# Optimization experiments

Hardware: AMD Instinct MI355X
Metric: run time of the kernel (lower is better)

Reference implementation:

```python
import jax, jax.numpy as jnp
import numpy as np

N = 50000   # num_embs = num nodes
E = 800000  # num edges
D = 256     # feature dim
L = 4       # num layers
EPS = 1e-5


def setup_inputs() -> dict:
    key = jax.random.key(0)
    ks = jax.random.split(key, 8)
    scale = 1.0 / np.sqrt(D)
    return {
        "x": jax.random.normal(ks[0], (N, D), dtype=jnp.float32),  # ignored by forward
        "edge_index": jax.random.randint(ks[1], (2, E), 0, N, dtype=jnp.int32),
        "edge_weight": jax.random.uniform(ks[2], (E,), dtype=jnp.float32),
        "emb_weight": jax.random.normal(ks[3], (N, D), dtype=jnp.float32),
        "ln_w": jnp.ones((L, D), dtype=jnp.float32),
        "ln_b": jnp.zeros((L, D), dtype=jnp.float32),
        "conv_w": jax.random.normal(ks[4], (L, D, D), dtype=jnp.float32) * scale,
        "conv_b": jnp.zeros((L, D), dtype=jnp.float32),
        "post_w": jax.random.normal(ks[5], (D, D), dtype=jnp.float32) * scale,
        "post_b": jnp.zeros((D,), dtype=jnp.float32),
    }


def _layer_norm(h, w, b):
    mu = jnp.mean(h, axis=-1, keepdims=True)
    var = jnp.mean(jnp.square(h - mu), axis=-1, keepdims=True)
    return (h - mu) * jax.lax.rsqrt(var + EPS) * w + b


def reference(x, edge_index, edge_weight, emb_weight, ln_w, ln_b, conv_w, conv_b, post_w, post_b):
    # GCNConv semantics (PyG defaults): add self-loops (weight 1), symmetric norm.
    loop = jnp.arange(N, dtype=edge_index.dtype)
    src = jnp.concatenate([edge_index[0], loop])
    dst = jnp.concatenate([edge_index[1], loop])
    w = jnp.concatenate([edge_weight, jnp.ones((N,), edge_weight.dtype)])
    deg = jax.ops.segment_sum(w, dst, num_segments=N)
    dinv = jnp.where(deg > 0, jax.lax.rsqrt(jnp.maximum(deg, 1e-12)), 0.0)
    coef = (dinv[src] * w * dinv[dst])[:, None]  # [E+N, 1]

    h = emb_weight  # forward ignores x; cond_emb is None
    for i in range(L):
        z = _layer_norm(h, ln_w[i], ln_b[i])          # node LayerNorm
        zw = z @ conv_w[i]                             # linear transform
        agg = jax.ops.segment_sum(coef * zw[src], dst, num_segments=N)
        z = agg + conv_b[i]
        z = jax.nn.gelu(z, approximate=False)          # torch GELU is exact
        h = z + h                                      # residual (dropout=0)
    return h @ post_w + post_b
```

## Files before the change

### kernel.cpp

```cpp
#include <hip/hip_runtime.h>
#include <hip/hip_bf16.h>

#define N_NODES 50000
#define N_EDGES 800000
#define DIM     256
#define NLAYERS 4
#define EPS     1e-5f
#define SCAN_B  196
#define MASK40  ((1ULL << 40) - 1)
#define EPACK_CAP (N_EDGES + 15 * N_NODES + 32)

typedef __bf16 bf16x8 __attribute__((ext_vector_type(8)));
typedef float  f32x4  __attribute__((ext_vector_type(4)));
typedef float  f32x2  __attribute__((ext_vector_type(2)));
typedef unsigned short u16x8 __attribute__((ext_vector_type(8)));

__device__ __forceinline__ unsigned short f2b(float f) {
    __hip_bfloat16 h = __float2bfloat16(f);
    return __builtin_bit_cast(unsigned short, h);
}
__device__ __forceinline__ float b2f(unsigned short u) {
    unsigned int v = ((unsigned int)u) << 16;
    return __builtin_bit_cast(float, v);
}
__device__ __forceinline__ float gelu_exact(float x) {
    return 0.5f * x * (1.0f + erff(x * 0.70710678118654752f));
}
__device__ __forceinline__ unsigned int pack_fp8x4(float a, float b, float c, float d) {
    int v = 0;
    v = __builtin_amdgcn_cvt_pk_fp8_f32(a, b, v, false);
    v = __builtin_amdgcn_cvt_pk_fp8_f32(c, d, v, true);
    return (unsigned int)v;
}

__global__ __launch_bounds__(256) void hist_kernel(const int* __restrict__ dst,
                                                   const float* __restrict__ w,
                                                   unsigned long long* __restrict__ cnt64,
                                                   int* __restrict__ rank) {
    int e = blockIdx.x * 256 + threadIdx.x;
    if (e >= N_EDGES) return;
    int d = dst[e];
    unsigned long long wfix = (unsigned long long)(w[e] * 4294967296.0f);
    unsigned long long old = atomicAdd(&cnt64[d], (1ULL << 40) | wfix);
    rank[e] = (int)(old >> 40);
}

__global__ __launch_bounds__(256) void scan_a_kernel(const unsigned long long* __restrict__ cnt64,
                                                     float* __restrict__ dinv,
                                                     int* __restrict__ bsum) {
    __shared__ int l[256];
    int i = blockIdx.x * 256 + threadIdx.x;
    int pc = 0;
    if (i < N_NODES) {
        unsigned long long v = cnt64[i];
        int cnt = (int)(v >> 40);
        float sw = (float)(v & MASK40) * 2.3283064365386963e-10f;
        dinv[i] = rsqrtf(1.0f + sw);
        pc = (cnt + 15) & ~15;
    }
    l[threadIdx.x] = pc;
    __syncthreads();
    for (int o = 128; o > 0; o >>= 1) {
        if (threadIdx.x < o) l[threadIdx.x] += l[threadIdx.x + o];
        __syncthreads();
    }
    if (threadIdx.x == 0) bsum[blockIdx.x] = l[0];
}

__global__ __launch_bounds__(256) void scan_b_kernel(const int* __restrict__ bsum,
                                                     int* __restrict__ boff,
                                                     int* __restrict__ rowptr) {
    __shared__ int l[256];
    int t = threadIdx.x;
    l[t] = (t < SCAN_B) ? bsum[t] : 0;
    __syncthreads();
    if (t == 0) {
        int run = 0;
        for (int j = 0; j < SCAN_B; ++j) { int v = l[j]; l[j] = run; run += v; }
        rowptr[N_NODES] = run;
    }
    __syncthreads();
    boff[t] = l[t];
}

__global__ __launch_bounds__(256) void scan_c_kernel(const unsigned long long* __restrict__ cnt64,
                                                     const int* __restrict__ boff,
                                                     int* __restrict__ rowptr) {
    __shared__ int l[256];
    int i = blockIdx.x * 256 + threadIdx.x;
    int pc = 0;
    if (i < N_NODES) {
        int cnt = (int)(cnt64[i] >> 40);
        pc = (cnt + 15) & ~15;
    }
    l[threadIdx.x] = pc;
    __syncthreads();
    if (threadIdx.x == 0) {
        int run = 0;
        for (int j = 0; j < 256; ++j) { int v = l[j]; l[j] = run; run += v; }
    }
    __syncthreads();
    if (i < N_NODES) rowptr[i] = boff[blockIdx.x] + l[threadIdx.x];
}

__global__ __launch_bounds__(256) void fill_kernel(const int* __restrict__ src,
                                                   const int* __restrict__ dst,
                                                   const float* __restrict__ w,
                                                   const float* __restrict__ dinv,
                                                   const int* __restrict__ rowptr,
                                                   const int* __restrict__ rank,
                                                   int2* __restrict__ epack) {
    int e = blockIdx.x * 256 + threadIdx.x;
    if (e >= N_EDGES) return;
    int s = src[e], d = dst[e];
    float c = dinv[s] * w[e] * dinv[d];
    int p = rowptr[d] + rank[e];
    epack[p] = make_int2(s << 8, __float_as_int(c));
}

__global__ __launch_bounds__(256) void convw_kernel(const float* __restrict__ conv_w,
                                                    const float* __restrict__ post_w,
                                                    unsigned short* __restrict__ Wt) {
    int idx = blockIdx.x * 256 + threadIdx.x;
    if (idx >= 5 * 65536) return;
    int m = idx >> 16;
    int r = idx & 65535;
    int n = r >> 8;
    int k = r & 255;
    float v = (m < 4) ? conv_w[m * 65536 + k * 256 + n] : post_w[k * 256 + n];
    Wt[idx] = f2b(v);
}

__global__ __launch_bounds__(256) void ln_cast_kernel(const float* __restrict__ H,
                                                      const float* __restrict__ lnw,
                                                      const float* __restrict__ lnb,
                                                      unsigned short* __restrict__ Z,
                                                      unsigned short* __restrict__ Hbf) {
    int row = blockIdx.x * 4 + (threadIdx.x >> 6);
    int lane = threadIdx.x & 63;
    const float4 x = *(const float4*)(H + (size_t)row * DIM + lane * 4);
    float s = x.x + x.y + x.z + x.w;
    for (int o = 32; o > 0; o >>= 1) s += __shfl_xor(s, o);
    float mu = s * (1.0f / DIM);
    float d0 = x.x - mu, d1 = x.y - mu, d2 = x.z - mu, d3 = x.w - mu;
    float v = d0 * d0 + d1 * d1 + d2 * d2 + d3 * d3;
    for (int o = 32; o > 0; o >>= 1) v += __shfl_xor(v, o);
    float rs = rsqrtf(v * (1.0f / DIM) + EPS);
    const float4 ww = *(const float4*)(lnw + lane * 4);
    const float4 bb = *(const float4*)(lnb + lane * 4);
    ushort4 o4;
    o4.x = f2b(d0 * rs * ww.x + bb.x);
    o4.y = f2b(d1 * rs * ww.y + bb.y);
    o4.z = f2b(d2 * rs * ww.z + bb.z);
    o4.w = f2b(d3 * rs * ww.w + bb.w);
    *(ushort4*)(Z + (size_t)row * DIM + lane * 4) = o4;
    ushort4 h4;
    h4.x = f2b(x.x); h4.y = f2b(x.y); h4.z = f2b(x.z); h4.w = f2b(x.w);
    *(ushort4*)(Hbf + (size_t)row * DIM + lane * 4) = h4;
}

template <int MODE>
__device__ __forceinline__ void gemm_body(const unsigned short* __restrict__ A,
                                          const unsigned short* __restrict__ Bt,
                                          void* __restrict__ Cout,
                                          const float* __restrict__ bias) {
    int tid = threadIdx.x;
    int wave = tid >> 6;
    int lane = tid & 63;
    int q = lane >> 4;
    int c16 = lane & 15;
    int mbase = blockIdx.x * 64;
    int cbase = wave * 64;

    const unsigned short* aptr[4];
    #pragma unroll
    for (int nt = 0; nt < 4; ++nt) {
        int row = mbase + nt * 16 + c16;
        if (row >= N_NODES) row = N_NODES - 1;
        aptr[nt] = A + (size_t)row * DIM;
    }
    const unsigned short* wptr[4];
    #pragma unroll
    for (int ct = 0; ct < 4; ++ct)
        wptr[ct] = Bt + (size_t)(cbase + ct * 16 + c16) * DIM;

    f32x4 acc[4][4] = {};
    #pragma unroll 1
    for (int k0 = 0; k0 < DIM; k0 += 32) {
        bf16x8 nf[4], wf[4];
        #pragma unroll
        for (int nt = 0; nt < 4; ++nt)
            nf[nt] = __builtin_bit_cast(bf16x8, *(const u16x8*)(aptr[nt] + k0 + q * 8));
        #pragma unroll
        for (int ct = 0; ct < 4; ++ct)
            wf[ct] = __builtin_bit_cast(bf16x8, *(const u16x8*)(wptr[ct] + k0 + q * 8));
        #pragma unroll
        for (int nt = 0; nt < 4; ++nt)
            #pragma unroll
            for (int ct = 0; ct < 4; ++ct)
                acc[nt][ct] = __builtin_amdgcn_mfma_f32_16x16x32_bf16(wf[ct], nf[nt], acc[nt][ct], 0, 0, 0);
    }

    float4 bb[4];
    if (MODE == 1) {
        #pragma unroll
        for (int ct = 0; ct < 4; ++ct)
            bb[ct] = *(const float4*)(bias + cbase + ct * 16 + q * 4);
    }
    #pragma unroll
    for (int nt = 0; nt < 4; ++nt) {
        int node = mbase + nt * 16 + c16;
        if (node >= N_NODES) continue;
        #pragma unroll
        for (int ct = 0; ct < 4; ++ct) {
            int chan = cbase + ct * 16 + q * 4;
            if (MODE == 0) {
                unsigned char* C = (unsigned char*)Cout;
                unsigned int pv = pack_fp8x4(acc[nt][ct][0], acc[nt][ct][1],
                                             acc[nt][ct][2], acc[nt][ct][3]);
                *(unsigned int*)(C + (size_t)node * DIM + chan) = pv;
            } else {
                float* C = (float*)Cout;
                float4 o;
                o.x = acc[nt][ct][0] + bb[ct].x;
                o.y = acc[nt][ct][1] + bb[ct].y;
                o.z = acc[nt][ct][2] + bb[ct].z;
                o.w = acc[nt][ct][3] + bb[ct].w;
                *(float4*)(C + (size_t)node * DIM + chan) = o;
            }
        }
    }
}

__global__ __launch_bounds__(256) void gemm_fp8_kernel(const unsigned short* __restrict__ A,
                                                       const unsigned short* __restrict__ Bt,
                                                       unsigned char* __restrict__ C) {
    gemm_body<0>(A, Bt, C, nullptr);
}

__global__ __launch_bounds__(256) void gemm_f32_kernel(const unsigned short* __restrict__ A,
                                                       const unsigned short* __restrict__ Bt,
                                                       float* __restrict__ C,
                                                       const float* __restrict__ bias) {
    gemm_body<1>(A, Bt, C, bias);
}

__global__ __launch_bounds__(256) void agg_kernel(const unsigned char* __restrict__ ZW,
                                                  unsigned short* __restrict__ Hbf,
                                                  const float* __restrict__ bias,
                                                  const int* __restrict__ rowptr,
                                                  const int2* __restrict__ epack,
                                                  const float* __restrict__ dinv,
                                                  const float* __restrict__ lnw,
                                                  const float* __restrict__ lnb,
                                                  unsigned short* __restrict__ Zout,
                                                  int doLN, int writeH) {
    int node = blockIdx.x * 4 + (threadIdx.x >> 6);
    int lane = threadIdx.x & 63;
    int g = lane >> 5;
    int colB = (lane & 31) * 8;

    float di = dinv[node];
    float scg = (g == 0) ? di * di : 0.0f;
    const uint2 zs = *(const uint2*)(ZW + (size_t)node * DIM + colB);
    float a[8];
    {
        f32x2 p0 = __builtin_amdgcn_cvt_pk_f32_fp8(zs.x, false);
        f32x2 p1 = __builtin_amdgcn_cvt_pk_f32_fp8(zs.x, true);
        f32x2 p2 = __builtin_amdgcn_cvt_pk_f32_fp8(zs.y, false);
        f32x2 p3 = __builtin_amdgcn_cvt_pk_f32_fp8(zs.y, true);
        a[0] = scg * p0.x; a[1] = scg * p0.y; a[2] = scg * p1.x; a[3] = scg * p1.y;
        a[4] = scg * p2.x; a[5] = scg * p2.y; a[6] = scg * p3.x; a[7] = scg * p3.y;
    }

    int e0 = rowptr[node], e1 = rowptr[node + 1];
    for (int e = e0; e < e1; e += 16) {
        const int2* pp = epack + e + 8 * g;
        const int4 q0 = *(const int4*)pp;
        const int4 q1 = *(const int4*)(pp + 2);
        const int4 q2 = *(const int4*)(pp + 4);
        const int4 q3 = *(const int4*)(pp + 6);
        const uint2 v0 = *(const uint2*)(ZW + q0.x + colB);
        const uint2 v1 = *(const uint2*)(ZW + q0.z + colB);
        const uint2 v2 = *(const uint2*)(ZW + q1.x + colB);
        const uint2 v3 = *(const uint2*)(ZW + q1.z + colB);
        const uint2 v4 = *(const uint2*)(ZW + q2.x + colB);
        const uint2 v5 = *(const uint2*)(ZW + q2.z + colB);
        const uint2 v6 = *(const uint2*)(ZW + q3.x + colB);
        const uint2 v7 = *(const uint2*)(ZW + q3.z + colB);
        float c0 = __int_as_float(q0.y), c1 = __int_as_float(q0.w);
        float c2 = __int_as_float(q1.y), c3 = __int_as_float(q1.w);
        float c4 = __int_as_float(q2.y), c5 = __int_as_float(q2.w);
        float c6 = __int_as_float(q3.y), c7 = __int_as_float(q3.w);
        #pragma unroll
        for (int h = 0; h < 8; ++h) {
            uint2 vv; float cc;
            switch (h) {
                case 0: vv = v0; cc = c0; break;
                case 1: vv = v1; cc = c1; break;
                case 2: vv = v2; cc = c2; break;
                case 3: vv = v3; cc = c3; break;
                case 4: vv = v4; cc = c4; break;
                case 5: vv = v5; cc = c5; break;
                case 6: vv = v6; cc = c6; break;
                default: vv = v7; cc = c7; break;
            }
            f32x2 p0 = __builtin_amdgcn_cvt_pk_f32_fp8(vv.x, false);
            f32x2 p1 = __builtin_amdgcn_cvt_pk_f32_fp8(vv.x, true);
            f32x2 p2 = __builtin_amdgcn_cvt_pk_f32_fp8(vv.y, false);
            f32x2 p3 = __builtin_amdgcn_cvt_pk_f32_fp8(vv.y, true);
            a[0] += cc * p0.x; a[1] += cc * p0.y;
            a[2] += cc * p1.x; a[3] += cc * p1.y;
            a[4] += cc * p2.x; a[5] += cc * p2.y;
            a[6] += cc * p3.x; a[7] += cc * p3.y;
        }
    }
    #pragma unroll
    for (int j = 0; j < 8; ++j) a[j] += __shfl_xor(a[j], 32);

    int col0 = (lane & 31) * 8;
    const float4 bb0 = *(const float4*)(bias + col0);
    const float4 bb1 = *(const float4*)(bias + col0 + 4);
    const u16x8 hv = *(const u16x8*)(Hbf + (size_t)node * DIM + col0);
    float o[8];
    o[0] = b2f(hv[0]) + gelu_exact(a[0] + bb0.x);
    o[1] = b2f(hv[1]) + gelu_exact(a[1] + bb0.y);
    o[2] = b2f(hv[2]) + gelu_exact(a[2] + bb0.z);
    o[3] = b2f(hv[3]) + gelu_exact(a[3] + bb0.w);
    o[4] = b2f(hv[4]) + gelu_exact(a[4] + bb1.x);
    o[5] = b2f(hv[5]) + gelu_exact(a[5] + bb1.y);
    o[6] = b2f(hv[6]) + gelu_exact(a[6] + bb1.z);
    o[7] = b2f(hv[7]) + gelu_exact(a[7] + bb1.w);

    if (writeH && g == 0) {
        u16x8 hw;
        #pragma unroll
        for (int j = 0; j < 8; ++j) hw[j] = f2b(o[j]);
        *(u16x8*)(Hbf + (size_t)node * DIM + col0) = hw;
    }

    float y[8];
    #pragma unroll
    for (int j = 0; j < 8; ++j) y[j] = o[j];
    if (doLN) {
        float s = 0.0f;
        #pragma unroll
        for (int j = 0; j < 8; ++j) s += o[j];
        for (int off = 16; off > 0; off >>= 1) s += __shfl_xor(s, off);
        float mu = s * (1.0f / DIM);
        float v = 0.0f;
        float d[8];
        #pragma unroll
        for (int j = 0; j < 8; ++j) { d[j] = o[j] - mu; v += d[j] * d[j]; }
        for (int off = 16; off > 0; off >>= 1) v += __shfl_xor(v, off);
        float rs = rsqrtf(v * (1.0f / DIM) + EPS);
        const float4 ww0 = *(const float4*)(lnw + col0);
        const float4 ww1 = *(const float4*)(lnw + col0 + 4);
        const float4 lb0 = *(const float4*)(lnb + col0);
        const float4 lb1 = *(const float4*)(lnb + col0 + 4);
        y[0] = d[0] * rs * ww0.x + lb0.x;
        y[1] = d[1] * rs * ww0.y + lb0.y;
        y[2] = d[2] * rs * ww0.z + lb0.z;
        y[3] = d[3] * rs * ww0.w + lb0.w;
        y[4] = d[4] * rs * ww1.x + lb1.x;
        y[5] = d[5] * rs * ww1.y + lb1.y;
        y[6] = d[6] * rs * ww1.z + lb1.z;
        y[7] = d[7] * rs * ww1.w + lb1.w;
    }
    if (g == 0) {
        u16x8 z;
        #pragma unroll
        for (int j = 0; j < 8; ++j) z[j] = f2b(y[j]);
        *(u16x8*)(Zout + (size_t)node * DIM + col0) = z;
    }
}

extern "C" void kernel_launch(void* const* d_in, const int* in_sizes, int n_in,
                              void* d_out, int out_size, void* d_ws, size_t ws_size,
                              hipStream_t stream) {
    const int*   ei     = (const int*)d_in[1];
    const int*   src    = ei;
    const int*   dst    = ei + N_EDGES;
    const float* ew     = (const float*)d_in[2];
    const float* emb    = (const float*)d_in[3];
    const float* ln_w   = (const float*)d_in[4];
    const float* ln_b   = (const float*)d_in[5];
    const float* conv_w = (const float*)d_in[6];
    const float* conv_b = (const float*)d_in[7];
    const float* post_w = (const float*)d_in[8];
    const float* post_b = (const float*)d_in[9];
    float* out = (float*)d_out;

    char* w = (char*)d_ws;
    size_t off = 0;
    auto alloc = [&](size_t bytes) -> char* {
        char* p = w + off;
        off += (bytes + 255) & ~(size_t)255;
        return p;
    };
    unsigned long long* cnt64 = (unsigned long long*)alloc((size_t)N_NODES * 8);
    float* dinv   = (float*)alloc((size_t)N_NODES * 4);
    int*   rank   = (int*)alloc((size_t)N_EDGES * 4);
    int*   rowptr = (int*)alloc((size_t)(N_NODES + 1) * 4);
    int*   bsum   = (int*)alloc(256 * 4);
    int*   boff   = (int*)alloc(256 * 4);
    int2*  epack  = (int2*)alloc((size_t)EPACK_CAP * 8);
    unsigned short* Wt  = (unsigned short*)alloc((size_t)5 * 65536 * 2);
    unsigned short* Z16 = (unsigned short*)alloc((size_t)N_NODES * DIM * 2);
    unsigned char*  ZW8 = (unsigned char*)alloc((size_t)N_NODES * DIM);
    unsigned short* Hbf = (unsigned short*)alloc((size_t)N_NODES * DIM * 2);

    hipMemsetAsync(cnt64, 0, (size_t)N_NODES * 8, stream);
    hipMemsetAsync(epack, 0, (size_t)EPACK_CAP * 8, stream);
    hist_kernel<<<N_EDGES / 256, 256, 0, stream>>>(dst, ew, cnt64, rank);
    scan_a_kernel<<<SCAN_B, 256, 0, stream>>>(cnt64, dinv, bsum);
    scan_b_kernel<<<1, 256, 0, stream>>>(bsum, boff, rowptr);
    scan_c_kernel<<<SCAN_B, 256, 0, stream>>>(cnt64, boff, rowptr);
    fill_kernel<<<N_EDGES / 256, 256, 0, stream>>>(src, dst, ew, dinv, rowptr, rank, epack);
    convw_kernel<<<(5 * 65536) / 256, 256, 0, stream>>>(conv_w, post_w, Wt);

    const int GEMM_GRID = (N_NODES + 63) / 64;
    ln_cast_kernel<<<N_NODES / 4, 256, 0, stream>>>(emb, ln_w, ln_b, Z16, Hbf);
    for (int l = 0; l < NLAYERS; ++l) {
        gemm_fp8_kernel<<<GEMM_GRID, 256, 0, stream>>>(Z16, Wt + (size_t)l * 65536, ZW8);
        int doLN = (l < NLAYERS - 1) ? 1 : 0;
        int writeH = (l < NLAYERS - 1) ? 1 : 0;
        const float* nlw = doLN ? (ln_w + (l + 1) * DIM) : nullptr;
        const float* nlb = doLN ? (ln_b + (l + 1) * DIM) : nullptr;
        agg_kernel<<<N_NODES / 4, 256, 0, stream>>>(ZW8, Hbf, conv_b + l * DIM,
                                                    rowptr, epack, dinv, nlw, nlb,
                                                    Z16, doLN, writeH);
    }
    gemm_f32_kernel<<<GEMM_GRID, 256, 0, stream>>>(Z16, Wt + (size_t)4 * 65536, out, post_b);
}
```

Before: 594.5 us.

## Aggregate before transform and fuse bias, GELU, residual, LayerNorm into GEMM epilogue

Reorders each layer to aggregate the LayerNorm output first (A·(Z·W) = (A·Z)·W), then runs the dense transform. Bias, exact GELU, the residual add and the next layer's LayerNorm move into the GEMM epilogue, with row statistics reduced through shared memory. The aggregation kernel now only gathers fp8 Z and writes bf16 sums, and the normalized activations are stored as fp8 instead of bf16. The intent is a lighter gather kernel and a smaller Z buffer. In exchange, the GEMM now reads bf16 aggregates, variance is computed as E[x²]−μ², and the extra fp8 quantization of Z before aggregation may cost accuracy.

```diff
diff --git a/kernel.cpp b/kernel.cpp
--- a/kernel.cpp
+++ b/kernel.cpp
@@ -14,6 +14,9 @@
 typedef float  f32x4  __attribute__((ext_vector_type(4)));
 typedef float  f32x2  __attribute__((ext_vector_type(2)));
 typedef unsigned short u16x8 __attribute__((ext_vector_type(8)));
+typedef unsigned short u16x4 __attribute__((ext_vector_type(4)));
+typedef int            i32x4 __attribute__((ext_vector_type(4)));
+typedef unsigned int   u32x2 __attribute__((ext_vector_type(2)));
 
 __device__ __forceinline__ unsigned short f2b(float f) {
     __hip_bfloat16 h = __float2bfloat16(f);
@@ -134,7 +137,7 @@
 __global__ __launch_bounds__(256) void ln_cast_kernel(const float* __restrict__ H,
                                                       const float* __restrict__ lnw,
                                                       const float* __restrict__ lnb,
-                                                      unsigned short* __restrict__ Z,
+                                                      unsigned char* __restrict__ Z8,
                                                       unsigned short* __restrict__ Hbf) {
     int row = blockIdx.x * 4 + (threadIdx.x >> 6);
     int lane = threadIdx.x & 63;
@@ -148,113 +151,21 @@
     float rs = rsqrtf(v * (1.0f / DIM) + EPS);
     const float4 ww = *(const float4*)(lnw + lane * 4);
     const float4 bb = *(const float4*)(lnb + lane * 4);
-    ushort4 o4;
-    o4.x = f2b(d0 * rs * ww.x + bb.x);
-    o4.y = f2b(d1 * rs * ww.y + bb.y);
-    o4.z = f2b(d2 * rs * ww.z + bb.z);
-    o4.w = f2b(d3 * rs * ww.w + bb.w);
-    *(ushort4*)(Z + (size_t)row * DIM + lane * 4) = o4;
+    float z0 = d0 * rs * ww.x + bb.x;
+    float z1 = d1 * rs * ww.y + bb.y;
+    float z2 = d2 * rs * ww.z + bb.z;
+    float z3 = d3 * rs * ww.w + bb.w;
+    *(unsigned int*)(Z8 + (size_t)row * DIM + lane * 4) = pack_fp8x4(z0, z1, z2, z3);
     ushort4 h4;
     h4.x = f2b(x.x); h4.y = f2b(x.y); h4.z = f2b(x.z); h4.w = f2b(x.w);
     *(ushort4*)(Hbf + (size_t)row * DIM + lane * 4) = h4;
 }
 
-template <int MODE>
-__device__ __forceinline__ void gemm_body(const unsigned short* __restrict__ A,
-                                          const unsigned short* __restrict__ Bt,
-                                          void* __restrict__ Cout,
-                                          const float* __restrict__ bias) {
-    int tid = threadIdx.x;
-    int wave = tid >> 6;
-    int lane = tid & 63;
-    int q = lane >> 4;
-    int c16 = lane & 15;
-    int mbase = blockIdx.x * 64;
-    int cbase = wave * 64;
-
-    const unsigned short* aptr[4];
-    #pragma unroll
-    for (int nt = 0; nt < 4; ++nt) {
-        int row = mbase + nt * 16 + c16;
-        if (row >= N_NODES) row = N_NODES - 1;
-        aptr[nt] = A + (size_t)row * DIM;
-    }
-    const unsigned short* wptr[4];
-    #pragma unroll
-    for (int ct = 0; ct < 4; ++ct)
-        wptr[ct] = Bt + (size_t)(cbase + ct * 16 + c16) * DIM;
-
-    f32x4 acc[4][4] = {};
-    #pragma unroll 1
-    for (int k0 = 0; k0 < DIM; k0 += 32) {
-        bf16x8 nf[4], wf[4];
-        #pragma unroll
-        for (int nt = 0; nt < 4; ++nt)
-            nf[nt] = __builtin_bit_cast(bf16x8, *(const u16x8*)(aptr[nt] + k0 + q * 8));
-        #pragma unroll
-        for (int ct = 0; ct < 4; ++ct)
-            wf[ct] = __builtin_bit_cast(bf16x8, *(const u16x8*)(wptr[ct] + k0 + q * 8));
-        #pragma unroll
-        for (int nt = 0; nt < 4; ++nt)
-            #pragma unroll
-            for (int ct = 0; ct < 4; ++ct)
-                acc[nt][ct] = __builtin_amdgcn_mfma_f32_16x16x32_bf16(wf[ct], nf[nt], acc[nt][ct], 0, 0, 0);
-    }
-
-    float4 bb[4];
-    if (MODE == 1) {
-        #pragma unroll
-        for (int ct = 0; ct < 4; ++ct)
-            bb[ct] = *(const float4*)(bias + cbase + ct * 16 + q * 4);
-    }
-    #pragma unroll
-    for (int nt = 0; nt < 4; ++nt) {
-        int node = mbase + nt * 16 + c16;
-        if (node >= N_NODES) continue;
-        #pragma unroll
-        for (int ct = 0; ct < 4; ++ct) {
-            int chan = cbase + ct * 16 + q * 4;
-            if (MODE == 0) {
-                unsigned char* C = (unsigned char*)Cout;
-                unsigned int pv = pack_fp8x4(acc[nt][ct][0], acc[nt][ct][1],
-                                             acc[nt][ct][2], acc[nt][ct][3]);
-                *(unsigned int*)(C + (size_t)node * DIM + chan) = pv;
-            } else {
-                float* C = (float*)Cout;
-                float4 o;
-                o.x = acc[nt][ct][0] + bb[ct].x;
-                o.y = acc[nt][ct][1] + bb[ct].y;
-                o.z = acc[nt][ct][2] + bb[ct].z;
-                o.w = acc[nt][ct][3] + bb[ct].w;
-                *(float4*)(C + (size_t)node * DIM + chan) = o;
-            }
-        }
-    }
-}
-
-__global__ __launch_bounds__(256) void gemm_fp8_kernel(const unsigned short* __restrict__ A,
-                                                       const unsigned short* __restrict__ Bt,
-                                                       unsigned char* __restrict__ C) {
-    gemm_body<0>(A, Bt, C, nullptr);
-}
-
-__global__ __launch_bounds__(256) void gemm_f32_kernel(const unsigned short* __restrict__ A,
-                                                       const unsigned short* __restrict__ Bt,
-                                                       float* __restrict__ C,
-                                                       const float* __restrict__ bias) {
-    gemm_body<1>(A, Bt, C, bias);
-}
-
-__global__ __launch_bounds__(256) void agg_kernel(const unsigned char* __restrict__ ZW,
-                                                  unsigned short* __restrict__ Hbf,
-                                                  const float* __restrict__ bias,
+__global__ __launch_bounds__(256) void agg_kernel(const unsigned char* __restrict__ Z8,
                                                   const int* __restrict__ rowptr,
                                                   const int2* __restrict__ epack,
                                                   const float* __restrict__ dinv,
-                                                  const float* __restrict__ lnw,
-                                                  const float* __restrict__ lnb,
-                                                  unsigned short* __restrict__ Zout,
-                                                  int doLN, int writeH) {
+                                                  unsigned short* __restrict__ AGG) {
     int node = blockIdx.x * 4 + (threadIdx.x >> 6);
     int lane = threadIdx.x & 63;
     int g = lane >> 5;
@@ -262,39 +173,38 @@
 
     float di = dinv[node];
     float scg = (g == 0) ? di * di : 0.0f;
-    const uint2 zs = *(const uint2*)(ZW + (size_t)node * DIM + colB);
-    float a[8];
+    const u32x2 zs = *(const u32x2*)(Z8 + (size_t)node * DIM + colB);
+    f32x2 a0, a1, a2, a3;
     {
-        f32x2 p0 = __builtin_amdgcn_cvt_pk_f32_fp8(zs.x, false);
-        f32x2 p1 = __builtin_amdgcn_cvt_pk_f32_fp8(zs.x, true);
-        f32x2 p2 = __builtin_amdgcn_cvt_pk_f32_fp8(zs.y, false);
-        f32x2 p3 = __builtin_amdgcn_cvt_pk_f32_fp8(zs.y, true);
-        a[0] = scg * p0.x; a[1] = scg * p0.y; a[2] = scg * p1.x; a[3] = scg * p1.y;
-        a[4] = scg * p2.x; a[5] = scg * p2.y; a[6] = scg * p3.x; a[7] = scg * p3.y;
+        f32x2 p0 = __builtin_amdgcn_cvt_pk_f32_fp8(zs[0], false);
+        f32x2 p1 = __builtin_amdgcn_cvt_pk_f32_fp8(zs[0], true);
+        f32x2 p2 = __builtin_amdgcn_cvt_pk_f32_fp8(zs[1], false);
+        f32x2 p3 = __builtin_amdgcn_cvt_pk_f32_fp8(zs[1], true);
+        a0 = scg * p0; a1 = scg * p1; a2 = scg * p2; a3 = scg * p3;
     }
 
     int e0 = rowptr[node], e1 = rowptr[node + 1];
     for (int e = e0; e < e1; e += 16) {
         const int2* pp = epack + e + 8 * g;
-        const int4 q0 = *(const int4*)pp;
-        const int4 q1 = *(const int4*)(pp + 2);
-        const int4 q2 = *(const int4*)(pp + 4);
-        const int4 q3 = *(const int4*)(pp + 6);
-        const uint2 v0 = *(const uint2*)(ZW + q0.x + colB);
-        const uint2 v1 = *(const uint2*)(ZW + q0.z + colB);
-        const uint2 v2 = *(const uint2*)(ZW + q1.x + colB);
-        const uint2 v3 = *(const uint2*)(ZW + q1.z + colB);
-        const uint2 v4 = *(const uint2*)(ZW + q2.x + colB);
-        const uint2 v5 = *(const uint2*)(ZW + q2.z + colB);
-        const uint2 v6 = *(const uint2*)(ZW + q3.x + colB);
-        const uint2 v7 = *(const uint2*)(ZW + q3.z + colB);
-        float c0 = __int_as_float(q0.y), c1 = __int_as_float(q0.w);
-        float c2 = __int_as_float(q1.y), c3 = __int_as_float(q1.w);
-        float c4 = __int_as_float(q2.y), c5 = __int_as_float(q2.w);
-        float c6 = __int_as_float(q3.y), c7 = __int_as_float(q3.w);
+        const i32x4 q0 = __builtin_nontemporal_load((const i32x4*)pp);
+        const i32x4 q1 = __builtin_nontemporal_load((const i32x4*)(pp + 2));
+        const i32x4 q2 = __builtin_nontemporal_load((const i32x4*)(pp + 4));
+        const i32x4 q3 = __builtin_nontemporal_load((const i32x4*)(pp + 6));
+        const u32x2 v0 = *(const u32x2*)(Z8 + q0[0] + colB);
+        const u32x2 v1 = *(const u32x2*)(Z8 + q0[2] + colB);
+        const u32x2 v2 = *(const u32x2*)(Z8 + q1[0] + colB);
+        const u32x2 v3 = *(const u32x2*)(Z8 + q1[2] + colB);
+        const u32x2 v4 = *(const u32x2*)(Z8 + q2[0] + colB);
+        const u32x2 v5 = *(const u32x2*)(Z8 + q2[2] + colB);
+        const u32x2 v6 = *(const u32x2*)(Z8 + q3[0] + colB);
+        const u32x2 v7 = *(const u32x2*)(Z8 + q3[2] + colB);
+        float c0 = __int_as_float(q0[1]), c1 = __int_as_float(q0[3]);
+        float c2 = __int_as_float(q1[1]), c3 = __int_as_float(q1[3]);
+        float c4 = __int_as_float(q2[1]), c5 = __int_as_float(q2[3]);
+        float c6 = __int_as_float(q3[1]), c7 = __int_as_float(q3[3]);
         #pragma unroll
         for (int h = 0; h < 8; ++h) {
-            uint2 vv; float cc;
+            u32x2 vv; float cc;
             switch (h) {
                 case 0: vv = v0; cc = c0; break;
                 case 1: vv = v1; cc = c1; break;
@@ -305,73 +215,208 @@
                 case 6: vv = v6; cc = c6; break;
                 default: vv = v7; cc = c7; break;
             }
-            f32x2 p0 = __builtin_amdgcn_cvt_pk_f32_fp8(vv.x, false);
-            f32x2 p1 = __builtin_amdgcn_cvt_pk_f32_fp8(vv.x, true);
-            f32x2 p2 = __builtin_amdgcn_cvt_pk_f32_fp8(vv.y, false);
-            f32x2 p3 = __builtin_amdgcn_cvt_pk_f32_fp8(vv.y, true);
-            a[0] += cc * p0.x; a[1] += cc * p0.y;
-            a[2] += cc * p1.x; a[3] += cc * p1.y;
-            a[4] += cc * p2.x; a[5] += cc * p2.y;
-            a[6] += cc * p3.x; a[7] += cc * p3.y;
-        }
-    }
+            f32x2 p0 = __builtin_amdgcn_cvt_pk_f32_fp8(vv[0], false);
+            f32x2 p1 = __builtin_amdgcn_cvt_pk_f32_fp8(vv[0], true);
+            f32x2 p2 = __builtin_amdgcn_cvt_pk_f32_fp8(vv[1], false);
+            f32x2 p3 = __builtin_amdgcn_cvt_pk_f32_fp8(vv[1], true);
+            a0 += cc * p0; a1 += cc * p1; a2 += cc * p2; a3 += cc * p3;
+        }
+    }
+    float a[8] = {a0[0], a0[1], a1[0], a1[1], a2[0], a2[1], a3[0], a3[1]};
     #pragma unroll
     for (int j = 0; j < 8; ++j) a[j] += __shfl_xor(a[j], 32);
 
-    int col0 = (lane & 31) * 8;
-    const float4 bb0 = *(const float4*)(bias + col0);
-    const float4 bb1 = *(const float4*)(bias + col0 + 4);
-    const u16x8 hv = *(const u16x8*)(Hbf + (size_t)node * DIM + col0);
-    float o[8];
-    o[0] = b2f(hv[0]) + gelu_exact(a[0] + bb0.x);
-    o[1] = b2f(hv[1]) + gelu_exact(a[1] + bb0.y);
-    o[2] = b2f(hv[2]) + gelu_exact(a[2] + bb0.z);
-    o[3] = b2f(hv[3]) + gelu_exact(a[3] + bb0.w);
-    o[4] = b2f(hv[4]) + gelu_exact(a[4] + bb1.x);
-    o[5] = b2f(hv[5]) + gelu_exact(a[5] + bb1.y);
-    o[6] = b2f(hv[6]) + gelu_exact(a[6] + bb1.z);
-    o[7] = b2f(hv[7]) + gelu_exact(a[7] + bb1.w);
-
-    if (writeH && g == 0) {
-        u16x8 hw;
-        #pragma unroll
-        for (int j = 0; j < 8; ++j) hw[j] = f2b(o[j]);
-        *(u16x8*)(Hbf + (size_t)node * DIM + col0) = hw;
-    }
-
-    float y[8];
-    #pragma unroll
-    for (int j = 0; j < 8; ++j) y[j] = o[j];
-    if (doLN) {
-        float s = 0.0f;
-        #pragma unroll
-        for (int j = 0; j < 8; ++j) s += o[j];
-        for (int off = 16; off > 0; off >>= 1) s += __shfl_xor(s, off);
-        float mu = s * (1.0f / DIM);
-        float v = 0.0f;
-        float d[8];
-        #pragma unroll
-        for (int j = 0; j < 8; ++j) { d[j] = o[j] - mu; v += d[j] * d[j]; }
-        for (int off = 16; off > 0; off >>= 1) v += __shfl_xor(v, off);
-        float rs = rsqrtf(v * (1.0f / DIM) + EPS);
-        const float4 ww0 = *(const float4*)(lnw + col0);
-        const float4 ww1 = *(const float4*)(lnw + col0 + 4);
-        const float4 lb0 = *(const float4*)(lnb + col0);
-        const float4 lb1 = *(const float4*)(lnb + col0 + 4);
-        y[0] = d[0] * rs * ww0.x + lb0.x;
-        y[1] = d[1] * rs * ww0.y + lb0.y;
-        y[2] = d[2] * rs * ww0.z + lb0.z;
-        y[3] = d[3] * rs * ww0.w + lb0.w;
-        y[4] = d[4] * rs * ww1.x + lb1.x;
-        y[5] = d[5] * rs * ww1.y + lb1.y;
-        y[6] = d[6] * rs * ww1.z + lb1.z;
-        y[7] = d[7] * rs * ww1.w + lb1.w;
-    }
     if (g == 0) {
         u16x8 z;
         #pragma unroll
-        for (int j = 0; j < 8; ++j) z[j] = f2b(y[j]);
-        *(u16x8*)(Zout + (size_t)node * DIM + col0) = z;
+        for (int j = 0; j < 8; ++j) z[j] = f2b(a[j]);
+        __builtin_nontemporal_store(z, (u16x8*)(AGG + (size_t)node * DIM + colB));
+    }
+}
+
+__global__ __launch_bounds__(256) void gemm_fused_kernel(const unsigned short* __restrict__ A,
+                                                         const unsigned short* __restrict__ Bt,
+                                                         const float* __restrict__ bias,
+                                                         unsigned short* __restrict__ Hbf,
+                                                         const float* __restrict__ lnw,
+                                                         const float* __restrict__ lnb,
+                                                         unsigned char* __restrict__ Z8,
+                                                         int doLN) {
+    __shared__ float s_sum[4][64];
+    __shared__ float s_sq[4][64];
+    int tid = threadIdx.x;
+    int wave = tid >> 6;
+    int lane = tid & 63;
+    int q = lane >> 4;
+    int c16 = lane & 15;
+    int mbase = blockIdx.x * 64;
+    int cbase = wave * 64;
+
+    int arow[4];
+    const unsigned short* aptr[4];
+    #pragma unroll
+    for (int nt = 0; nt < 4; ++nt) {
+        int row = mbase + nt * 16 + c16;
+        arow[nt] = (row >= N_NODES) ? (N_NODES - 1) : row;
+        aptr[nt] = A + (size_t)arow[nt] * DIM;
+    }
+    const unsigned short* wptr[4];
+    #pragma unroll
+    for (int ct = 0; ct < 4; ++ct)
+        wptr[ct] = Bt + (size_t)(cbase + ct * 16 + c16) * DIM;
+
+    f32x4 acc[4][4] = {};
+    #pragma unroll 1
+    for (int k0 = 0; k0 < DIM; k0 += 32) {
+        bf16x8 nf[4], wf[4];
+        #pragma unroll
+        for (int nt = 0; nt < 4; ++nt)
+            nf[nt] = __builtin_bit_cast(bf16x8, *(const u16x8*)(aptr[nt] + k0 + q * 8));
+        #pragma unroll
+        for (int ct = 0; ct < 4; ++ct)
+            wf[ct] = __builtin_bit_cast(bf16x8, *(const u16x8*)(wptr[ct] + k0 + q * 8));
+        #pragma unroll
+        for (int nt = 0; nt < 4; ++nt)
+            #pragma unroll
+            for (int ct = 0; ct < 4; ++ct)
+                acc[nt][ct] = __builtin_amdgcn_mfma_f32_16x16x32_bf16(wf[ct], nf[nt], acc[nt][ct], 0, 0, 0);
+    }
+
+    float psum[4], psq[4];
+    #pragma unroll
+    for (int nt = 0; nt < 4; ++nt) {
+        psum[nt] = 0.0f; psq[nt] = 0.0f;
+        #pragma unroll
+        for (int ct = 0; ct < 4; ++ct) {
+            int chan = cbase + ct * 16 + q * 4;
+            const f32x4 bb = *(const f32x4*)(bias + chan);
+            const u16x4 hv = __builtin_nontemporal_load(
+                (const u16x4*)(Hbf + (size_t)arow[nt] * DIM + chan));
+            #pragma unroll
+            for (int j = 0; j < 4; ++j) {
+                float v = acc[nt][ct][j] + bb[j];
+                float hn = gelu_exact(v) + b2f(hv[j]);
+                acc[nt][ct][j] = hn;
+                psum[nt] += hn;
+                psq[nt] += hn * hn;
+            }
+        }
+    }
+
+    float mu[4], rs[4];
+    if (doLN) {
+        #pragma unroll
+        for (int nt = 0; nt < 4; ++nt) {
+            psum[nt] += __shfl_xor(psum[nt], 16);
+            psum[nt] += __shfl_xor(psum[nt], 32);
+            psq[nt]  += __shfl_xor(psq[nt], 16);
+            psq[nt]  += __shfl_xor(psq[nt], 32);
+        }
+        if (q == 0) {
+            #pragma unroll
+            for (int nt = 0; nt < 4; ++nt) {
+                s_sum[wave][nt * 16 + c16] = psum[nt];
+                s_sq[wave][nt * 16 + c16]  = psq[nt];
+            }
+        }
+        __syncthreads();
+        #pragma unroll
+        for (int nt = 0; nt < 4; ++nt) {
+            int li = nt * 16 + c16;
+            float ts = s_sum[0][li] + s_sum[1][li] + s_sum[2][li] + s_sum[3][li];
+            float tq = s_sq[0][li] + s_sq[1][li] + s_sq[2][li] + s_sq[3][li];
+            float m = ts * (1.0f / DIM);
+            float var = fmaxf(tq * (1.0f / DIM) - m * m, 0.0f);
+            mu[nt] = m;
+            rs[nt] = rsqrtf(var + EPS);
+        }
+    }
+
+    #pragma unroll
+    for (int nt = 0; nt < 4; ++nt) {
+        int node = mbase + nt * 16 + c16;
+        if (node >= N_NODES) continue;
+        #pragma unroll
+        for (int ct = 0; ct < 4; ++ct) {
+            int chan = cbase + ct * 16 + q * 4;
+            u16x4 hw;
+            hw[0] = f2b(acc[nt][ct][0]);
+            hw[1] = f2b(acc[nt][ct][1]);
+            hw[2] = f2b(acc[nt][ct][2]);
+            hw[3] = f2b(acc[nt][ct][3]);
+            __builtin_nontemporal_store(hw, (u16x4*)(Hbf + (size_t)node * DIM + chan));
+            if (doLN) {
+                const f32x4 ww = *(const f32x4*)(lnw + chan);
+                const f32x4 lb = *(const f32x4*)(lnb + chan);
+                float y0 = (acc[nt][ct][0] - mu[nt]) * rs[nt] * ww[0] + lb[0];
+                float y1 = (acc[nt][ct][1] - mu[nt]) * rs[nt] * ww[1] + lb[1];
+                float y2 = (acc[nt][ct][2] - mu[nt]) * rs[nt] * ww[2] + lb[2];
+                float y3 = (acc[nt][ct][3] - mu[nt]) * rs[nt] * ww[3] + lb[3];
+                *(unsigned int*)(Z8 + (size_t)node * DIM + chan) = pack_fp8x4(y0, y1, y2, y3);
+            }
+        }
+    }
+}
+
+__global__ __launch_bounds__(256) void gemm_out_kernel(const unsigned short* __restrict__ A,
+                                                       const unsigned short* __restrict__ Bt,
+                                                       float* __restrict__ C,
+                                                       const float* __restrict__ bias) {
+    int tid = threadIdx.x;
+    int wave = tid >> 6;
+    int lane = tid & 63;
+    int q = lane >> 4;
+    int c16 = lane & 15;
+    int mbase = blockIdx.x * 64;
+    int cbase = wave * 64;
+
+    const unsigned short* aptr[4];
+    #pragma unroll
+    for (int nt = 0; nt < 4; ++nt) {
+        int row = mbase + nt * 16 + c16;
+        if (row >= N_NODES) row = N_NODES - 1;
+        aptr[nt] = A + (size_t)row * DIM;
+    }
+    const unsigned short* wptr[4];
+    #pragma unroll
+    for (int ct = 0; ct < 4; ++ct)
+        wptr[ct] = Bt + (size_t)(cbase + ct * 16 + c16) * DIM;
+
+    f32x4 acc[4][4] = {};
+    #pragma unroll 1
+    for (int k0 = 0; k0 < DIM; k0 += 32) {
+        bf16x8 nf[4], wf[4];
+        #pragma unroll
+        for (int nt = 0; nt < 4; ++nt)
+            nf[nt] = __builtin_bit_cast(bf16x8, *(const u16x8*)(aptr[nt] + k0 + q * 8));
+        #pragma unroll
+        for (int ct = 0; ct < 4; ++ct)
+            wf[ct] = __builtin_bit_cast(bf16x8, *(const u16x8*)(wptr[ct] + k0 + q * 8));
+        #pragma unroll
+        for (int nt = 0; nt < 4; ++nt)
+            #pragma unroll
+            for (int ct = 0; ct < 4; ++ct)
+                acc[nt][ct] = __builtin_amdgcn_mfma_f32_16x16x32_bf16(wf[ct], nf[nt], acc[nt][ct], 0, 0, 0);
+    }
+
+    float4 bb[4];
+    #pragma unroll
+    for (int ct = 0; ct < 4; ++ct)
+        bb[ct] = *(const float4*)(bias + cbase + ct * 16 + q * 4);
+    #pragma unroll
+    for (int nt = 0; nt < 4; ++nt) {
+        int node = mbase + nt * 16 + c16;
+        if (node >= N_NODES) continue;
+        #pragma unroll
+        for (int ct = 0; ct < 4; ++ct) {
+            int chan = cbase + ct * 16 + q * 4;
+            float4 o;
+            o.x = acc[nt][ct][0] + bb[ct].x;
+            o.y = acc[nt][ct][1] + bb[ct].y;
+            o.z = acc[nt][ct][2] + bb[ct].z;
+            o.w = acc[nt][ct][3] + bb[ct].w;
+            *(float4*)(C + (size_t)node * DIM + chan) = o;
+        }
     }
 }
 
@@ -405,10 +450,10 @@
     int*   bsum   = (int*)alloc(256 * 4);
     int*   boff   = (int*)alloc(256 * 4);
     int2*  epack  = (int2*)alloc((size_t)EPACK_CAP * 8);
-    unsigned short* Wt  = (unsigned short*)alloc((size_t)5 * 65536 * 2);
-    unsigned short* Z16 = (unsigned short*)alloc((size_t)N_NODES * DIM * 2);
-    unsigned char*  ZW8 = (unsigned char*)alloc((size_t)N_NODES * DIM);
-    unsigned short* Hbf = (unsigned short*)alloc((size_t)N_NODES * DIM * 2);
+    unsigned short* Wt    = (unsigned short*)alloc((size_t)5 * 65536 * 2);
+    unsigned short* AGG16 = (unsigned short*)alloc((size_t)N_NODES * DIM * 2);
+    unsigned char*  Z8    = (unsigned char*)alloc((size_t)N_NODES * DIM);
+    unsigned short* Hbf   = (unsigned short*)alloc((size_t)N_NODES * DIM * 2);
 
     hipMemsetAsync(cnt64, 0, (size_t)N_NODES * 8, stream);
     hipMemsetAsync(epack, 0, (size_t)EPACK_CAP * 8, stream);
@@ -420,16 +465,15 @@
     convw_kernel<<<(5 * 65536) / 256, 256, 0, stream>>>(conv_w, post_w, Wt);
 
     const int GEMM_GRID = (N_NODES + 63) / 64;
-    ln_cast_kernel<<<N_NODES / 4, 256, 0, stream>>>(emb, ln_w, ln_b, Z16, Hbf);
+    ln_cast_kernel<<<N_NODES / 4, 256, 0, stream>>>(emb, ln_w, ln_b, Z8, Hbf);
     for (int l = 0; l < NLAYERS; ++l) {
-        gemm_fp8_kernel<<<GEMM_GRID, 256, 0, stream>>>(Z16, Wt + (size_t)l * 65536, ZW8);
+        agg_kernel<<<N_NODES / 4, 256, 0, stream>>>(Z8, rowptr, epack, dinv, AGG16);
         int doLN = (l < NLAYERS - 1) ? 1 : 0;
-        int writeH = (l < NLAYERS - 1) ? 1 : 0;
-        const float* nlw = doLN ? (ln_w + (l + 1) * DIM) : nullptr;
-        const float* nlb = doLN ? (ln_b + (l + 1) * DIM) : nullptr;
-        agg_kernel<<<N_NODES / 4, 256, 0, stream>>>(ZW8, Hbf, conv_b + l * DIM,
-                                                    rowptr, epack, dinv, nlw, nlb,
-                                                    Z16, doLN, writeH);
-    }
-    gemm_f32_kernel<<<GEMM_GRID, 256, 0, stream>>>(Z16, Wt + (size_t)4 * 65536, out, post_b);
-}
+        const float* nlw = doLN ? (ln_w + (l + 1) * DIM) : ln_w;
+        const float* nlb = doLN ? (ln_b + (l + 1) * DIM) : ln_b;
+        gemm_fused_kernel<<<GEMM_GRID, 256, 0, stream>>>(AGG16, Wt + (size_t)l * 65536,
+                                                         conv_b + (size_t)l * DIM, Hbf,
+                                                         nlw, nlb, Z8, doLN);
+    }
+    gemm_out_kernel<<<GEMM_GRID, 256, 0, stream>>>(Hbf, Wt + (size_t)4 * 65536, out, post_b);
+}
```

After: 713.2 us. 1.2x slower.
